# Kernel tuning notes

Measured on AMD Instinct MI355X. Metric: run time of the kernel, lower is better.

The kernel has to match this reference:

```python
import jax, jax.numpy as jnp
import numpy as np

D_K = 64
MASK_FILL = -1e9


def setup_inputs() -> dict:
    key = jax.random.key(0)
    kq, kk, kv, km = jax.random.split(key, 4)
    B, H, S, D = 2, 16, 2048, D_K
    q = jax.random.normal(kq, (B, H, S, D), dtype=jnp.float32)
    k = jax.random.normal(kk, (B, H, D, S), dtype=jnp.float32)  # pre-transposed keys
    v = jax.random.normal(kv, (B, H, S, D), dtype=jnp.float32)
    mask = jax.random.randint(km, (B, H, S, S), 0, 2).astype(jnp.bool_)
    return {"q": q, "k": k, "v": v, "mask": mask}


def reference(q, k, v, mask):
    # scores: [B, H, S, S] = q @ k (k already [B,H,D,S])
    scores = jnp.einsum("bhsd,bhdt->bhst", q, k) / jnp.sqrt(jnp.float32(D_K))
    scores = jnp.where(mask, MASK_FILL, scores)
    attn = jax.nn.softmax(scores, axis=-1)
    context = jnp.einsum("bhst,bhtd->bhsd", attn, v)
    return (context, attn)
```

## Files before the change

### kernel.cpp

```cpp
#include <hip/hip_runtime.h>

#define S_LEN    2048
#define DK       64
#define N_BH     32
#define ROWS     16
#define NTHREADS 512

typedef float          f32x4  __attribute__((ext_vector_type(4)));
typedef int            i32x4  __attribute__((ext_vector_type(4)));
typedef short          bf16x8 __attribute__((ext_vector_type(8)));
typedef unsigned short u16x8  __attribute__((ext_vector_type(8)));
typedef unsigned int   u32x4  __attribute__((ext_vector_type(4)));

__device__ __forceinline__ unsigned short f2bf(float f) {
    unsigned u = __builtin_bit_cast(unsigned, f);
    u += 0x7fffu + ((u >> 16) & 1u);
    return (unsigned short)(u >> 16);
}
__device__ __forceinline__ float bf2f(unsigned short h) {
    unsigned u = ((unsigned)h) << 16;
    return __builtin_bit_cast(float, u);
}
__device__ __forceinline__ unsigned pack_bf2(float a, float b) {
    return (unsigned)f2bf(a) | ((unsigned)f2bf(b) << 16);
}

__global__ void prep_q(const float* __restrict__ q, unsigned short* __restrict__ Q2) {
    const int bq = blockIdx.x;
    const int tx = threadIdx.x;
    const int ks = tx >> 6, g = (tx >> 4) & 3, m = tx & 15;
    const long row = ((long)(bq >> 7) * S_LEN + (bq & 127) * 16 + m);
    const float* p = q + row * DK + ks * 32 + g * 8;
    f32x4 x0 = *(const f32x4*)p, x1 = *(const f32x4*)(p + 4);
    u16x8 o;
    o[0]=f2bf(x0.x); o[1]=f2bf(x0.y); o[2]=f2bf(x0.z); o[3]=f2bf(x0.w);
    o[4]=f2bf(x1.x); o[5]=f2bf(x1.y); o[6]=f2bf(x1.z); o[7]=f2bf(x1.w);
    *(u16x8*)(Q2 + (long)bq * 1024 + tx * 8) = o;
}

__global__ void prep_k(const float* __restrict__ k, unsigned short* __restrict__ K2) {
    __shared__ float t[64][65];
    const int bh = blockIdx.x >> 5, s0 = (blockIdx.x & 31) << 6;
    const int tx = threadIdx.x;
    const float* kb = k + (long)bh * DK * S_LEN;
    #pragma unroll
    for (int i = 0; i < 16; ++i) {
        const int d = (i << 2) + (tx >> 6), s = tx & 63;
        t[d][s] = kb[(long)d * S_LEN + s0 + s];
    }
    __syncthreads();
    #pragma unroll
    for (int it = 0; it < 2; ++it) {
        const int flat = it * 256 + tx;
        const int m = flat & 15, g = (flat >> 4) & 3, ks = (flat >> 6) & 1, t16g = flat >> 7;
        const int sl = t16g * 16 + m;
        const int d0 = ks * 32 + g * 8;
        u16x8 o;
        #pragma unroll
        for (int j = 0; j < 8; ++j) o[j] = f2bf(t[d0 + j][sl]);
        const long idx = ((((long)(bh * 128 + (s0 >> 4) + t16g) * 2 + ks) * 4 + g) * 16 + m) * 8;
        *(u16x8*)(K2 + idx) = o;
    }
}

__global__ void prep_v(const float* __restrict__ v, unsigned short* __restrict__ V2) {
    __shared__ float t[64][65];
    const int bh = blockIdx.x >> 5, s0 = (blockIdx.x & 31) << 6;
    const int tx = threadIdx.x;
    #pragma unroll
    for (int i = 0; i < 16; ++i) {
        const int s = (i << 2) + (tx >> 6), d = tx & 63;
        t[s][d] = v[((long)bh * S_LEN + s0 + s) * DK + d];
    }
    __syncthreads();
    #pragma unroll
    for (int it = 0; it < 2; ++it) {
        const int flat = it * 256 + tx;
        const int d = flat & 63, tbl = flat >> 6;
        u16x8 o;
        #pragma unroll
        for (int j = 0; j < 8; ++j) o[j] = f2bf(t[tbl * 8 + j][d]);
        const long idx = (((long)(bh * 256 + (s0 >> 3) + tbl) * 64) + d) * 8;
        *(u16x8*)(V2 + idx) = o;
    }
}

template <bool WS>
__global__ __launch_bounds__(NTHREADS, 4)
void sdpa_main(const float* __restrict__ q, const float* __restrict__ k,
               const float* __restrict__ v, const int* __restrict__ mask,
               const unsigned short* __restrict__ Q2,
               const unsigned short* __restrict__ K2,
               const unsigned short* __restrict__ V2,
               float* __restrict__ ctx, float* __restrict__ attn)
{
    __shared__ float rowsum[ROWS];
    __shared__ float ctxlds[ROWS * DK];

    const int bid  = blockIdx.x;
    const int bh   = bid & (N_BH - 1);
    const int qt   = bid >> 5;
    const int tid  = threadIdx.x;
    const int wave = tid >> 6;
    const int lane = tid & 63;
    const int m    = lane & 15;
    const int g    = lane >> 4;
    const long rowbase = (long)bh * S_LEN + qt * ROWS;
    const int tw   = wave << 8;

    if (tid < ROWS) rowsum[tid] = 0.0f;
    for (int i = tid; i < ROWS * DK; i += NTHREADS) ctxlds[i] = 0.0f;
    __syncthreads();

    unsigned long long mbits = 0ull;
    {
        const int* mbase = mask + rowbase * S_LEN + tw + 4 * lane;
        #pragma unroll
        for (int r = 0; r < 16; ++r) {
            const i32x4 mk = __builtin_nontemporal_load((const i32x4*)(mbase + (long)r * S_LEN));
            const unsigned nib = (mk.x ? 1u : 0u) | (mk.y ? 2u : 0u)
                               | (mk.z ? 4u : 0u) | (mk.w ? 8u : 0u);
            mbits |= ((unsigned long long)nib) << (r * 4);
        }
    }

    bf16x8 qfrag[2];
    if (WS) {
        const unsigned short* qp = Q2 + ((long)((bh * 128 + qt) * 2) << 9) + (lane << 3);
        qfrag[0] = *(const bf16x8*)qp;
        qfrag[1] = *(const bf16x8*)(qp + 512);
    } else {
        const float* qp = q + (rowbase + m) * DK;
        #pragma unroll
        for (int ks = 0; ks < 2; ++ks) {
            const float* p = qp + ks * 32 + g * 8;
            f32x4 x0 = *(const f32x4*)p, x1 = *(const f32x4*)(p + 4);
            qfrag[ks][0]=(short)f2bf(x0.x); qfrag[ks][1]=(short)f2bf(x0.y);
            qfrag[ks][2]=(short)f2bf(x0.z); qfrag[ks][3]=(short)f2bf(x0.w);
            qfrag[ks][4]=(short)f2bf(x1.x); qfrag[ks][5]=(short)f2bf(x1.y);
            qfrag[ks][6]=(short)f2bf(x1.z); qfrag[ks][7]=(short)f2bf(x1.w);
        }
    }

    unsigned long long lanemask = 0ull;
    {
        const unsigned mlo = (unsigned)mbits, mhi = (unsigned)(mbits >> 32);
        #pragma unroll
        for (int kt = 0; kt < 8; ++kt) {
            const int sA = kt * 8 + g * 2, sB = sA + 1;
            const unsigned aLo = (unsigned)__shfl((int)mlo, sA);
            const unsigned aHi = (unsigned)__shfl((int)mhi, sA);
            const unsigned bLo = (unsigned)__shfl((int)mlo, sB);
            const unsigned bHi = (unsigned)__shfl((int)mhi, sB);
            const unsigned long long A = ((unsigned long long)aHi << 32) | aLo;
            const unsigned long long B = ((unsigned long long)bHi << 32) | bLo;
            const unsigned byt = (unsigned)((A >> (4 * m)) & 0xFull)
                               | ((unsigned)((B >> (4 * m)) & 0xFull) << 4);
            lanemask |= ((unsigned long long)byt) << (8 * kt);
        }
    }

    const int srcA = ((g & 1) << 5) + m;
    const int srcB = srcA + 16;
    const int hi   = g >> 1;

    u32x4 AF[8];
    f32x4 cacc0 = {0,0,0,0}, cacc1 = {0,0,0,0}, cacc2 = {0,0,0,0}, cacc3 = {0,0,0,0};
    float rsum = 0.0f;

    #pragma unroll
    for (int kt = 0; kt < 8; ++kt) {
        unsigned pk0e, pk1e, pk0o, pk1o;
        #pragma unroll
        for (int h = 0; h < 2; ++h) {
            f32x4 acc = {0.f, 0.f, 0.f, 0.f};
            #pragma unroll
            for (int ks = 0; ks < 2; ++ks) {
                bf16x8 kfrag;
                if (WS) {
                    const unsigned short* kp = K2
                        + (((long)(bh * 128 + wave * 16 + 2 * kt + h) * 2 + ks) << 9)
                        + (lane << 3);
                    kfrag = *(const bf16x8*)kp;
                } else {
                    const int t0 = tw + ((2 * kt + h) << 4);
                    const int tk = t0 + m;
                    const float* kp = k + (long)bh * DK * S_LEN + (long)(ks * 32 + g * 8) * S_LEN + tk;
                    #pragma unroll
                    for (int j = 0; j < 8; ++j) kfrag[j] = (short)f2bf(kp[(long)j * S_LEN]);
                }
                acc = __builtin_amdgcn_mfma_f32_16x16x32_bf16(kfrag, qfrag[ks], acc, 0, 0, 0);
            }
            const float e0 = __expf(acc[0] * 0.125f);
            const float e1 = __expf(acc[1] * 0.125f);
            const float e2 = __expf(acc[2] * 0.125f);
            const float e3 = __expf(acc[3] * 0.125f);
            if (h == 0) { pk0e = pack_bf2(e0, e1); pk1e = pack_bf2(e2, e3); }
            else        { pk0o = pack_bf2(e0, e1); pk1o = pack_bf2(e2, e3); }
        }
        const unsigned a0e = (unsigned)__shfl((int)pk0e, srcA);
        const unsigned a0o = (unsigned)__shfl((int)pk0o, srcA);
        const unsigned a1e = (unsigned)__shfl((int)pk1e, srcA);
        const unsigned a1o = (unsigned)__shfl((int)pk1o, srcA);
        const unsigned a2e = (unsigned)__shfl((int)pk0e, srcB);
        const unsigned a2o = (unsigned)__shfl((int)pk0o, srcB);
        const unsigned a3e = (unsigned)__shfl((int)pk1e, srcB);
        const unsigned a3o = (unsigned)__shfl((int)pk1o, srcB);
        u32x4 wv = { hi ? a0o : a0e, hi ? a1o : a1e,
                     hi ? a2o : a2e, hi ? a3o : a3e };
        const unsigned mb = (unsigned)(lanemask >> (8 * kt)) & 0xFFu;
        if (mb & 1u)   wv.x &= 0xFFFF0000u;
        if (mb & 2u)   wv.x &= 0x0000FFFFu;
        if (mb & 4u)   wv.y &= 0xFFFF0000u;
        if (mb & 8u)   wv.y &= 0x0000FFFFu;
        if (mb & 16u)  wv.z &= 0xFFFF0000u;
        if (mb & 32u)  wv.z &= 0x0000FFFFu;
        if (mb & 64u)  wv.w &= 0xFFFF0000u;
        if (mb & 128u) wv.w &= 0x0000FFFFu;
        AF[kt] = wv;
        rsum += ((bf2f((unsigned short)(wv.x & 0xFFFF)) + bf2f((unsigned short)(wv.x >> 16)))
               + (bf2f((unsigned short)(wv.y & 0xFFFF)) + bf2f((unsigned short)(wv.y >> 16))))
              + ((bf2f((unsigned short)(wv.z & 0xFFFF)) + bf2f((unsigned short)(wv.z >> 16)))
               + (bf2f((unsigned short)(wv.w & 0xFFFF)) + bf2f((unsigned short)(wv.w >> 16))));
        const bf16x8 af = __builtin_bit_cast(bf16x8, wv);
        #pragma unroll
        for (int dt = 0; dt < 4; ++dt) {
            bf16x8 bfv;
            if (WS) {
                const unsigned short* vp2 = V2
                    + ((((long)(bh * 256 + (wave << 5) + (kt << 2) + g)) << 6) + dt * 16 + m) * 8;
                bfv = *(const bf16x8*)vp2;
            } else {
                const int tb = tw + (kt << 5) + (g << 3);
                const float* vp = v + ((long)bh * S_LEN + tb) * DK + dt * 16 + m;
                #pragma unroll
                for (int j = 0; j < 8; ++j) bfv[j] = (short)f2bf(vp[j * DK]);
            }
            if      (dt == 0) cacc0 = __builtin_amdgcn_mfma_f32_16x16x32_bf16(af, bfv, cacc0, 0, 0, 0);
            else if (dt == 1) cacc1 = __builtin_amdgcn_mfma_f32_16x16x32_bf16(af, bfv, cacc1, 0, 0, 0);
            else if (dt == 2) cacc2 = __builtin_amdgcn_mfma_f32_16x16x32_bf16(af, bfv, cacc2, 0, 0, 0);
            else              cacc3 = __builtin_amdgcn_mfma_f32_16x16x32_bf16(af, bfv, cacc3, 0, 0, 0);
        }
    }

    rsum += __shfl_xor(rsum, 16);
    rsum += __shfl_xor(rsum, 32);
    if (lane < 16) atomicAdd(&rowsum[lane], rsum);
    #pragma unroll
    for (int i = 0; i < 4; ++i) {
        atomicAdd(&ctxlds[(4 * g + i) * DK +  0 + m], cacc0[i]);
        atomicAdd(&ctxlds[(4 * g + i) * DK + 16 + m], cacc1[i]);
        atomicAdd(&ctxlds[(4 * g + i) * DK + 32 + m], cacc2[i]);
        atomicAdd(&ctxlds[(4 * g + i) * DK + 48 + m], cacc3[i]);
    }
    __syncthreads();

    {
        const float rinv = 1.0f / rowsum[m];
        float* aout = attn + (rowbase + m) * (long)S_LEN;
        #pragma unroll
        for (int kt = 0; kt < 8; ++kt) {
            const u32x4 wv = AF[kt];
            const int tb = tw + (kt << 5) + (g << 3);
            f32x4 o0 = { bf2f((unsigned short)(wv.x & 0xFFFF)) * rinv,
                         bf2f((unsigned short)(wv.x >> 16))    * rinv,
                         bf2f((unsigned short)(wv.y & 0xFFFF)) * rinv,
                         bf2f((unsigned short)(wv.y >> 16))    * rinv };
            f32x4 o1 = { bf2f((unsigned short)(wv.z & 0xFFFF)) * rinv,
                         bf2f((unsigned short)(wv.z >> 16))    * rinv,
                         bf2f((unsigned short)(wv.w & 0xFFFF)) * rinv,
                         bf2f((unsigned short)(wv.w >> 16))    * rinv };
            __builtin_nontemporal_store(o0, (f32x4*)(aout + tb));
            __builtin_nontemporal_store(o1, (f32x4*)(aout + tb + 4));
        }
    }

    #pragma unroll
    for (int i = tid; i < ROWS * DK; i += NTHREADS) {
        const int rr = i >> 6, dd = i & 63;
        ctx[(rowbase + rr) * DK + dd] = ctxlds[i] / rowsum[rr];
    }
}

extern "C" void kernel_launch(void* const* d_in, const int* in_sizes, int n_in,
                              void* d_out, int out_size, void* d_ws, size_t ws_size,
                              hipStream_t stream)
{
    const float* q    = (const float*)d_in[0];
    const float* k    = (const float*)d_in[1];
    const float* v    = (const float*)d_in[2];
    const int*   mask = (const int*)d_in[3];

    float* ctx  = (float*)d_out;
    float* attn = ctx + (size_t)N_BH * S_LEN * DK;

    const size_t nel = (size_t)N_BH * S_LEN * DK;
    const bool use_ws = ws_size >= nel * 3 * sizeof(unsigned short);
    unsigned short* Q2 = (unsigned short*)d_ws;
    unsigned short* K2 = Q2 + nel;
    unsigned short* V2 = K2 + nel;

    const int nblocks = N_BH * (S_LEN / ROWS);

    if (use_ws) {
        prep_q<<<N_BH * 128, 128, 0, stream>>>(q, Q2);
        prep_k<<<N_BH * (S_LEN / 64), 256, 0, stream>>>(k, K2);
        prep_v<<<N_BH * (S_LEN / 64), 256, 0, stream>>>(v, V2);
        sdpa_main<true><<<nblocks, NTHREADS, 0, stream>>>(q, k, v, mask, Q2, K2, V2, ctx, attn);
    } else {
        sdpa_main<false><<<nblocks, NTHREADS, 0, stream>>>(q, k, v, mask,
                                                           nullptr, nullptr, nullptr, ctx, attn);
    }
}
```

Baseline: 459.1 us.

## Tile 128 query rows per block with LDS-staged K/V and two-pass softmax

Each block now handles 128 query rows (16 per wave) instead of 16, and streams K and V in 128-key tiles through swizzled LDS buffers with register prefetch. The first pass computes exp scores and row sums, and the second pass recomputes QK, normalises, writes attn and accumulates context. This removes the cross-wave LDS atomics and the repeated global K/V reads of the old per-wave key split. The cost is recomputing QK in the second pass, a larger LDS footprint that lowers occupancy, and more barriers. Mask bits are cached in LDS between the passes.

```diff
diff --git a/kernel.cpp b/kernel.cpp
--- a/kernel.cpp
+++ b/kernel.cpp
@@ -3,14 +3,14 @@
 #define S_LEN    2048
 #define DK       64
 #define N_BH     32
-#define ROWS     16
 #define NTHREADS 512
 
-typedef float          f32x4  __attribute__((ext_vector_type(4)));
-typedef int            i32x4  __attribute__((ext_vector_type(4)));
-typedef short          bf16x8 __attribute__((ext_vector_type(8)));
-typedef unsigned short u16x8  __attribute__((ext_vector_type(8)));
-typedef unsigned int   u32x4  __attribute__((ext_vector_type(4)));
+typedef float              f32x4  __attribute__((ext_vector_type(4)));
+typedef int                i32x4  __attribute__((ext_vector_type(4)));
+typedef short              bf16x8 __attribute__((ext_vector_type(8)));
+typedef unsigned short     u16x8  __attribute__((ext_vector_type(8)));
+typedef unsigned int       u32x4  __attribute__((ext_vector_type(4)));
+typedef unsigned long long u64;
 
 __device__ __forceinline__ unsigned short f2bf(float f) {
     unsigned u = __builtin_bit_cast(unsigned, f);
@@ -35,7 +35,7 @@
     u16x8 o;
     o[0]=f2bf(x0.x); o[1]=f2bf(x0.y); o[2]=f2bf(x0.z); o[3]=f2bf(x0.w);
     o[4]=f2bf(x1.x); o[5]=f2bf(x1.y); o[6]=f2bf(x1.z); o[7]=f2bf(x1.w);
-    *(u16x8*)(Q2 + (long)bq * 1024 + tx * 8) = o;
+    *(u16x8*)(Q2 + (long)bq * 1024 + (ks * 512) + ((g * 16 + m) * 8)) = o;
 }
 
 __global__ void prep_k(const float* __restrict__ k, unsigned short* __restrict__ K2) {
@@ -51,15 +51,15 @@
     __syncthreads();
     #pragma unroll
     for (int it = 0; it < 2; ++it) {
-        const int flat = it * 256 + tx;
-        const int m = flat & 15, g = (flat >> 4) & 3, ks = (flat >> 6) & 1, t16g = flat >> 7;
-        const int sl = t16g * 16 + m;
-        const int d0 = ks * 32 + g * 8;
+        const int f = it * 256 + tx;
+        const int tl = f >> 3, d0 = f & 7;
+        const int tg = s0 + tl;
+        const int p = tg >> 7, tp = tg & 127;
         u16x8 o;
         #pragma unroll
-        for (int j = 0; j < 8; ++j) o[j] = f2bf(t[d0 + j][sl]);
-        const long idx = ((((long)(bh * 128 + (s0 >> 4) + t16g) * 2 + ks) * 4 + g) * 16 + m) * 8;
-        *(u16x8*)(K2 + idx) = o;
+        for (int j = 0; j < 8; ++j) o[j] = f2bf(t[d0 * 8 + j][tl]);
+        const int idx = (tp * 64 + d0 * 8) ^ ((tp & 7) << 3);
+        *(u16x8*)(K2 + ((long)(bh * 16 + p) << 13) + idx) = o;
     }
 }
 
@@ -75,13 +75,15 @@
     __syncthreads();
     #pragma unroll
     for (int it = 0; it < 2; ++it) {
-        const int flat = it * 256 + tx;
-        const int d = flat & 63, tbl = flat >> 6;
+        const int f = it * 256 + tx;
+        const int d = f >> 3, t8 = (f & 7) * 8;
+        const int tg8 = s0 + t8;
+        const int p = tg8 >> 7, tp8 = tg8 & 127;
         u16x8 o;
         #pragma unroll
-        for (int j = 0; j < 8; ++j) o[j] = f2bf(t[tbl * 8 + j][d]);
-        const long idx = (((long)(bh * 256 + (s0 >> 3) + tbl) * 64) + d) * 8;
-        *(u16x8*)(V2 + idx) = o;
+        for (int j = 0; j < 8; ++j) o[j] = f2bf(t[t8 + j][d]);
+        const int idx = (d * 128 + tp8) ^ ((d & 7) << 3);
+        *(u16x8*)(V2 + ((long)(bh * 16 + p) << 13) + idx) = o;
     }
 }
 
@@ -94,8 +96,9 @@
                const unsigned short* __restrict__ V2,
                float* __restrict__ ctx, float* __restrict__ attn)
 {
-    __shared__ float rowsum[ROWS];
-    __shared__ float ctxlds[ROWS * DK];
+    __shared__ unsigned short Kbuf[8192];
+    __shared__ unsigned short Vbuf[8192];
+    __shared__ u64 Mlds[4096];
 
     const int bid  = blockIdx.x;
     const int bh   = bid & (N_BH - 1);
@@ -105,28 +108,11 @@
     const int lane = tid & 63;
     const int m    = lane & 15;
     const int g    = lane >> 4;
-    const long rowbase = (long)bh * S_LEN + qt * ROWS;
-    const int tw   = wave << 8;
-
-    if (tid < ROWS) rowsum[tid] = 0.0f;
-    for (int i = tid; i < ROWS * DK; i += NTHREADS) ctxlds[i] = 0.0f;
-    __syncthreads();
-
-    unsigned long long mbits = 0ull;
-    {
-        const int* mbase = mask + rowbase * S_LEN + tw + 4 * lane;
-        #pragma unroll
-        for (int r = 0; r < 16; ++r) {
-            const i32x4 mk = __builtin_nontemporal_load((const i32x4*)(mbase + (long)r * S_LEN));
-            const unsigned nib = (mk.x ? 1u : 0u) | (mk.y ? 2u : 0u)
-                               | (mk.z ? 4u : 0u) | (mk.w ? 8u : 0u);
-            mbits |= ((unsigned long long)nib) << (r * 4);
-        }
-    }
+    const long rowbase = (long)bh * S_LEN + qt * 128 + wave * 16;
 
     bf16x8 qfrag[2];
     if (WS) {
-        const unsigned short* qp = Q2 + ((long)((bh * 128 + qt) * 2) << 9) + (lane << 3);
+        const unsigned short* qp = Q2 + ((long)(bh * 128 + qt * 8 + wave) << 10) + (lane << 3);
         qfrag[0] = *(const bf16x8*)qp;
         qfrag[1] = *(const bf16x8*)(qp + 512);
     } else {
@@ -142,54 +128,21 @@
         }
     }
 
-    unsigned long long lanemask = 0ull;
-    {
-        const unsigned mlo = (unsigned)mbits, mhi = (unsigned)(mbits >> 32);
-        #pragma unroll
-        for (int kt = 0; kt < 8; ++kt) {
-            const int sA = kt * 8 + g * 2, sB = sA + 1;
-            const unsigned aLo = (unsigned)__shfl((int)mlo, sA);
-            const unsigned aHi = (unsigned)__shfl((int)mhi, sA);
-            const unsigned bLo = (unsigned)__shfl((int)mlo, sB);
-            const unsigned bHi = (unsigned)__shfl((int)mhi, sB);
-            const unsigned long long A = ((unsigned long long)aHi << 32) | aLo;
-            const unsigned long long B = ((unsigned long long)bHi << 32) | bLo;
-            const unsigned byt = (unsigned)((A >> (4 * m)) & 0xFull)
-                               | ((unsigned)((B >> (4 * m)) & 0xFull) << 4);
-            lanemask |= ((unsigned long long)byt) << (8 * kt);
-        }
-    }
-
     const int srcA = ((g & 1) << 5) + m;
     const int srcB = srcA + 16;
     const int hi   = g >> 1;
 
-    u32x4 AF[8];
-    f32x4 cacc0 = {0,0,0,0}, cacc1 = {0,0,0,0}, cacc2 = {0,0,0,0}, cacc3 = {0,0,0,0};
-    float rsum = 0.0f;
-
-    #pragma unroll
-    for (int kt = 0; kt < 8; ++kt) {
+    auto qk_chunk = [&](int ct16a) -> u32x4 {
         unsigned pk0e, pk1e, pk0o, pk1o;
         #pragma unroll
         for (int h = 0; h < 2; ++h) {
+            const int tl = (ct16a + h) * 16 + m;
             f32x4 acc = {0.f, 0.f, 0.f, 0.f};
             #pragma unroll
             for (int ks = 0; ks < 2; ++ks) {
-                bf16x8 kfrag;
-                if (WS) {
-                    const unsigned short* kp = K2
-                        + (((long)(bh * 128 + wave * 16 + 2 * kt + h) * 2 + ks) << 9)
-                        + (lane << 3);
-                    kfrag = *(const bf16x8*)kp;
-                } else {
-                    const int t0 = tw + ((2 * kt + h) << 4);
-                    const int tk = t0 + m;
-                    const float* kp = k + (long)bh * DK * S_LEN + (long)(ks * 32 + g * 8) * S_LEN + tk;
-                    #pragma unroll
-                    for (int j = 0; j < 8; ++j) kfrag[j] = (short)f2bf(kp[(long)j * S_LEN]);
-                }
-                acc = __builtin_amdgcn_mfma_f32_16x16x32_bf16(kfrag, qfrag[ks], acc, 0, 0, 0);
+                const int idx = (tl * 64 + ks * 32 + g * 8) ^ ((tl & 7) << 3);
+                const bf16x8 kf = *(const bf16x8*)&Kbuf[idx];
+                acc = __builtin_amdgcn_mfma_f32_16x16x32_bf16(kf, qfrag[ks], acc, 0, 0, 0);
             }
             const float e0 = __expf(acc[0] * 0.125f);
             const float e1 = __expf(acc[1] * 0.125f);
@@ -208,7 +161,10 @@
         const unsigned a3o = (unsigned)__shfl((int)pk1o, srcB);
         u32x4 wv = { hi ? a0o : a0e, hi ? a1o : a1e,
                      hi ? a2o : a2e, hi ? a3o : a3e };
-        const unsigned mb = (unsigned)(lanemask >> (8 * kt)) & 0xFFu;
+        return wv;
+    };
+
+    auto apply_mask = [&](u32x4 wv, unsigned mb) -> u32x4 {
         if (mb & 1u)   wv.x &= 0xFFFF0000u;
         if (mb & 2u)   wv.x &= 0x0000FFFFu;
         if (mb & 4u)   wv.y &= 0xFFFF0000u;
@@ -217,51 +173,176 @@
         if (mb & 32u)  wv.z &= 0x0000FFFFu;
         if (mb & 64u)  wv.w &= 0xFFFF0000u;
         if (mb & 128u) wv.w &= 0x0000FFFFu;
-        AF[kt] = wv;
-        rsum += ((bf2f((unsigned short)(wv.x & 0xFFFF)) + bf2f((unsigned short)(wv.x >> 16)))
-               + (bf2f((unsigned short)(wv.y & 0xFFFF)) + bf2f((unsigned short)(wv.y >> 16))))
-              + ((bf2f((unsigned short)(wv.z & 0xFFFF)) + bf2f((unsigned short)(wv.z >> 16)))
-               + (bf2f((unsigned short)(wv.w & 0xFFFF)) + bf2f((unsigned short)(wv.w >> 16))));
-        const bf16x8 af = __builtin_bit_cast(bf16x8, wv);
-        #pragma unroll
-        for (int dt = 0; dt < 4; ++dt) {
-            bf16x8 bfv;
+        return wv;
+    };
+
+    auto mask_burst = [&](int c) -> u64 {
+        u64 mb = 0;
+        const int* mp = mask + rowbase * (long)S_LEN + c * 256 + 4 * lane;
+        #pragma unroll
+        for (int r = 0; r < 16; ++r) {
+            const i32x4 mk = __builtin_nontemporal_load((const i32x4*)(mp + (long)r * S_LEN));
+            const unsigned nib = (mk.x ? 1u : 0u) | (mk.y ? 2u : 0u)
+                               | (mk.z ? 4u : 0u) | (mk.w ? 8u : 0u);
+            mb |= ((u64)nib) << (r * 4);
+        }
+        return mb;
+    };
+
+    auto redist = [&](u64 mbits) -> u64 {
+        u64 lm = 0;
+        const unsigned mlo = (unsigned)mbits, mhi = (unsigned)(mbits >> 32);
+        #pragma unroll
+        for (int kt = 0; kt < 8; ++kt) {
+            const int sA = kt * 8 + g * 2, sB = sA + 1;
+            const unsigned aLo = (unsigned)__shfl((int)mlo, sA);
+            const unsigned aHi = (unsigned)__shfl((int)mhi, sA);
+            const unsigned bLo = (unsigned)__shfl((int)mlo, sB);
+            const unsigned bHi = (unsigned)__shfl((int)mhi, sB);
+            const u64 A = ((u64)aHi << 32) | aLo;
+            const u64 B = ((u64)bHi << 32) | bLo;
+            const unsigned byt = (unsigned)((A >> (4 * m)) & 0xFull)
+                               | ((unsigned)((B >> (4 * m)) & 0xFull) << 4);
+            lm |= ((u64)byt) << (8 * kt);
+        }
+        return lm;
+    };
+
+    float rsum = 0.0f;
+    u64 lm = redist(mask_burst(0));
+    u16x8 kst0, kst1;
+    if (WS) {
+        const unsigned short* src = K2 + ((long)(bh * 16) << 13) + (tid << 3);
+        kst0 = *(const u16x8*)src;
+        kst1 = *(const u16x8*)(src + 4096);
+    } else {
+        const int f0 = tid, f1 = 512 + tid;
+        const int tl0 = f0 >> 3, d00 = (f0 & 7) * 8, tl1 = f1 >> 3, d01 = (f1 & 7) * 8;
+        #pragma unroll
+        for (int j = 0; j < 8; ++j) kst0[j] = f2bf(k[((long)bh * DK + d00 + j) * S_LEN + tl0]);
+        #pragma unroll
+        for (int j = 0; j < 8; ++j) kst1[j] = f2bf(k[((long)bh * DK + d01 + j) * S_LEN + tl1]);
+    }
+    for (int p = 0; p < 16; ++p) {
+        const int c = p >> 1;
+        __syncthreads();
+        {
             if (WS) {
-                const unsigned short* vp2 = V2
-                    + ((((long)(bh * 256 + (wave << 5) + (kt << 2) + g)) << 6) + dt * 16 + m) * 8;
-                bfv = *(const bf16x8*)vp2;
+                *(u16x8*)&Kbuf[tid * 8]        = kst0;
+                *(u16x8*)&Kbuf[4096 + tid * 8] = kst1;
             } else {
-                const int tb = tw + (kt << 5) + (g << 3);
-                const float* vp = v + ((long)bh * S_LEN + tb) * DK + dt * 16 + m;
-                #pragma unroll
-                for (int j = 0; j < 8; ++j) bfv[j] = (short)f2bf(vp[j * DK]);
-            }
-            if      (dt == 0) cacc0 = __builtin_amdgcn_mfma_f32_16x16x32_bf16(af, bfv, cacc0, 0, 0, 0);
-            else if (dt == 1) cacc1 = __builtin_amdgcn_mfma_f32_16x16x32_bf16(af, bfv, cacc1, 0, 0, 0);
-            else if (dt == 2) cacc2 = __builtin_amdgcn_mfma_f32_16x16x32_bf16(af, bfv, cacc2, 0, 0, 0);
-            else              cacc3 = __builtin_amdgcn_mfma_f32_16x16x32_bf16(af, bfv, cacc3, 0, 0, 0);
-        }
+                const int f0 = tid, f1 = 512 + tid;
+                const int tl0 = f0 >> 3, d00 = (f0 & 7) * 8, tl1 = f1 >> 3, d01 = (f1 & 7) * 8;
+                *(u16x8*)&Kbuf[(tl0 * 64 + d00) ^ ((tl0 & 7) << 3)] = kst0;
+                *(u16x8*)&Kbuf[(tl1 * 64 + d01) ^ ((tl1 & 7) << 3)] = kst1;
+            }
+        }
+        if (p < 15) {
+            if (WS) {
+                const unsigned short* src = K2 + ((long)(bh * 16 + p + 1) << 13) + (tid << 3);
+                kst0 = *(const u16x8*)src;
+                kst1 = *(const u16x8*)(src + 4096);
+            } else {
+                const int f0 = tid, f1 = 512 + tid;
+                const int tl0 = (p + 1) * 128 + (f0 >> 3), d00 = (f0 & 7) * 8;
+                const int tl1 = (p + 1) * 128 + (f1 >> 3), d01 = (f1 & 7) * 8;
+                #pragma unroll
+                for (int j = 0; j < 8; ++j) kst0[j] = f2bf(k[((long)bh * DK + d00 + j) * S_LEN + tl0]);
+                #pragma unroll
+                for (int j = 0; j < 8; ++j) kst1[j] = f2bf(k[((long)bh * DK + d01 + j) * S_LEN + tl1]);
+            }
+        }
+        __syncthreads();
+        if ((p & 1) == 0) Mlds[(wave << 9) + (c << 6) + lane] = lm;
+        const int b0 = (p & 1) * 4;
+        #pragma unroll
+        for (int cc = 0; cc < 4; ++cc) {
+            u32x4 wv = qk_chunk(cc * 2);
+            const unsigned mb = (unsigned)(lm >> (8 * (b0 + cc))) & 0xFFu;
+            wv = apply_mask(wv, mb);
+            rsum += ((bf2f((unsigned short)(wv.x & 0xFFFF)) + bf2f((unsigned short)(wv.x >> 16)))
+                   + (bf2f((unsigned short)(wv.y & 0xFFFF)) + bf2f((unsigned short)(wv.y >> 16))))
+                  + ((bf2f((unsigned short)(wv.z & 0xFFFF)) + bf2f((unsigned short)(wv.z >> 16)))
+                   + (bf2f((unsigned short)(wv.w & 0xFFFF)) + bf2f((unsigned short)(wv.w >> 16))));
+        }
+        if ((p & 1) == 1 && p < 15) lm = redist(mask_burst(c + 1));
     }
 
     rsum += __shfl_xor(rsum, 16);
     rsum += __shfl_xor(rsum, 32);
-    if (lane < 16) atomicAdd(&rowsum[lane], rsum);
-    #pragma unroll
-    for (int i = 0; i < 4; ++i) {
-        atomicAdd(&ctxlds[(4 * g + i) * DK +  0 + m], cacc0[i]);
-        atomicAdd(&ctxlds[(4 * g + i) * DK + 16 + m], cacc1[i]);
-        atomicAdd(&ctxlds[(4 * g + i) * DK + 32 + m], cacc2[i]);
-        atomicAdd(&ctxlds[(4 * g + i) * DK + 48 + m], cacc3[i]);
-    }
-    __syncthreads();
-
-    {
-        const float rinv = 1.0f / rowsum[m];
-        float* aout = attn + (rowbase + m) * (long)S_LEN;
-        #pragma unroll
-        for (int kt = 0; kt < 8; ++kt) {
-            const u32x4 wv = AF[kt];
-            const int tb = tw + (kt << 5) + (g << 3);
+    const float rinv = 1.0f / rsum;
+
+    f32x4 cacc0 = {0,0,0,0}, cacc1 = {0,0,0,0}, cacc2 = {0,0,0,0}, cacc3 = {0,0,0,0};
+    u16x8 vst0, vst1;
+    if (WS) {
+        const unsigned short* ks_ = K2 + ((long)(bh * 16) << 13) + (tid << 3);
+        kst0 = *(const u16x8*)ks_;  kst1 = *(const u16x8*)(ks_ + 4096);
+        const unsigned short* vs_ = V2 + ((long)(bh * 16) << 13) + (tid << 3);
+        vst0 = *(const u16x8*)vs_;  vst1 = *(const u16x8*)(vs_ + 4096);
+    } else {
+        const int f0 = tid, f1 = 512 + tid;
+        const int tl0 = f0 >> 3, d00 = (f0 & 7) * 8, tl1 = f1 >> 3, d01 = (f1 & 7) * 8;
+        #pragma unroll
+        for (int j = 0; j < 8; ++j) kst0[j] = f2bf(k[((long)bh * DK + d00 + j) * S_LEN + tl0]);
+        #pragma unroll
+        for (int j = 0; j < 8; ++j) kst1[j] = f2bf(k[((long)bh * DK + d01 + j) * S_LEN + tl1]);
+        const int dv0 = f0 >> 3, t80 = (f0 & 7) * 8, dv1 = f1 >> 3, t81 = (f1 & 7) * 8;
+        #pragma unroll
+        for (int j = 0; j < 8; ++j) vst0[j] = f2bf(v[((long)bh * S_LEN + t80 + j) * DK + dv0]);
+        #pragma unroll
+        for (int j = 0; j < 8; ++j) vst1[j] = f2bf(v[((long)bh * S_LEN + t81 + j) * DK + dv1]);
+    }
+    float* aout = attn + (rowbase + m) * (long)S_LEN;
+    for (int p = 0; p < 16; ++p) {
+        const int c = p >> 1;
+        __syncthreads();
+        {
+            if (WS) {
+                *(u16x8*)&Kbuf[tid * 8]        = kst0;
+                *(u16x8*)&Kbuf[4096 + tid * 8] = kst1;
+                *(u16x8*)&Vbuf[tid * 8]        = vst0;
+                *(u16x8*)&Vbuf[4096 + tid * 8] = vst1;
+            } else {
+                const int f0 = tid, f1 = 512 + tid;
+                const int tl0 = f0 >> 3, d00 = (f0 & 7) * 8, tl1 = f1 >> 3, d01 = (f1 & 7) * 8;
+                *(u16x8*)&Kbuf[(tl0 * 64 + d00) ^ ((tl0 & 7) << 3)] = kst0;
+                *(u16x8*)&Kbuf[(tl1 * 64 + d01) ^ ((tl1 & 7) << 3)] = kst1;
+                const int dv0 = f0 >> 3, t80 = (f0 & 7) * 8, dv1 = f1 >> 3, t81 = (f1 & 7) * 8;
+                *(u16x8*)&Vbuf[(dv0 * 128 + t80) ^ ((dv0 & 7) << 3)] = vst0;
+                *(u16x8*)&Vbuf[(dv1 * 128 + t81) ^ ((dv1 & 7) << 3)] = vst1;
+            }
+        }
+        if (p < 15) {
+            if (WS) {
+                const unsigned short* ks_ = K2 + ((long)(bh * 16 + p + 1) << 13) + (tid << 3);
+                kst0 = *(const u16x8*)ks_;  kst1 = *(const u16x8*)(ks_ + 4096);
+                const unsigned short* vs_ = V2 + ((long)(bh * 16 + p + 1) << 13) + (tid << 3);
+                vst0 = *(const u16x8*)vs_;  vst1 = *(const u16x8*)(vs_ + 4096);
+            } else {
+                const int f0 = tid, f1 = 512 + tid;
+                const int tl0 = (p+1)*128 + (f0 >> 3), d00 = (f0 & 7) * 8;
+                const int tl1 = (p+1)*128 + (f1 >> 3), d01 = (f1 & 7) * 8;
+                #pragma unroll
+                for (int j = 0; j < 8; ++j) kst0[j] = f2bf(k[((long)bh * DK + d00 + j) * S_LEN + tl0]);
+                #pragma unroll
+                for (int j = 0; j < 8; ++j) kst1[j] = f2bf(k[((long)bh * DK + d01 + j) * S_LEN + tl1]);
+                const int dv0 = f0 >> 3, t80 = (p+1)*128 + (f0 & 7) * 8;
+                const int dv1 = f1 >> 3, t81 = (p+1)*128 + (f1 & 7) * 8;
+                #pragma unroll
+                for (int j = 0; j < 8; ++j) vst0[j] = f2bf(v[((long)bh * S_LEN + t80 + j) * DK + dv0]);
+                #pragma unroll
+                for (int j = 0; j < 8; ++j) vst1[j] = f2bf(v[((long)bh * S_LEN + t81 + j) * DK + dv1]);
+            }
+        }
+        __syncthreads();
+        const u64 lm2 = Mlds[(wave << 9) + (c << 6) + lane];
+        const int b0 = (p & 1) * 4;
+        #pragma unroll
+        for (int cc = 0; cc < 4; ++cc) {
+            u32x4 wv = qk_chunk(cc * 2);
+            const unsigned mb = (unsigned)(lm2 >> (8 * (b0 + cc))) & 0xFFu;
+            wv = apply_mask(wv, mb);
+            const int tb = p * 128 + cc * 32 + g * 8;
             f32x4 o0 = { bf2f((unsigned short)(wv.x & 0xFFFF)) * rinv,
                          bf2f((unsigned short)(wv.x >> 16))    * rinv,
                          bf2f((unsigned short)(wv.y & 0xFFFF)) * rinv,
@@ -272,13 +353,28 @@
                          bf2f((unsigned short)(wv.w >> 16))    * rinv };
             __builtin_nontemporal_store(o0, (f32x4*)(aout + tb));
             __builtin_nontemporal_store(o1, (f32x4*)(aout + tb + 4));
+            const bf16x8 af = __builtin_bit_cast(bf16x8, wv);
+            #pragma unroll
+            for (int dt = 0; dt < 4; ++dt) {
+                const int d = dt * 16 + m;
+                const int idx = (d * 128 + cc * 32 + g * 8) ^ ((d & 7) << 3);
+                const bf16x8 bfv = *(const bf16x8*)&Vbuf[idx];
+                if      (dt == 0) cacc0 = __builtin_amdgcn_mfma_f32_16x16x32_bf16(af, bfv, cacc0, 0, 0, 0);
+                else if (dt == 1) cacc1 = __builtin_amdgcn_mfma_f32_16x16x32_bf16(af, bfv, cacc1, 0, 0, 0);
+                else if (dt == 2) cacc2 = __builtin_amdgcn_mfma_f32_16x16x32_bf16(af, bfv, cacc2, 0, 0, 0);
+                else              cacc3 = __builtin_amdgcn_mfma_f32_16x16x32_bf16(af, bfv, cacc3, 0, 0, 0);
+            }
         }
     }
 
     #pragma unroll
-    for (int i = tid; i < ROWS * DK; i += NTHREADS) {
-        const int rr = i >> 6, dd = i & 63;
-        ctx[(rowbase + rr) * DK + dd] = ctxlds[i] / rowsum[rr];
+    for (int i = 0; i < 4; ++i) {
+        const float ri = __shfl(rinv, 4 * g + i);
+        float* cp = ctx + (rowbase + 4 * g + i) * DK + m;
+        cp[ 0] = cacc0[i] * ri;
+        cp[16] = cacc1[i] * ri;
+        cp[32] = cacc2[i] * ri;
+        cp[48] = cacc3[i] * ri;
     }
 }
 
@@ -300,7 +396,7 @@
     unsigned short* K2 = Q2 + nel;
     unsigned short* V2 = K2 + nel;
 
-    const int nblocks = N_BH * (S_LEN / ROWS);
+    const int nblocks = N_BH * (S_LEN / 128);
 
     if (use_ws) {
         prep_q<<<N_BH * 128, 128, 0, stream>>>(q, Q2);
```

New measurement: 565.0 us. 1.23x slower.

## Two-pass softmax: recompute QK scores to stream attn output, drop Q prep kernel

Applied to the files above, without the earlier changes.

Splits the main kernel into two passes. The first computes QK^T and exp only to get row sums. The second recomputes the scores and writes normalized attention straight out while doing the PV MFMAs, so the bf16 probabilities no longer sit in registers (AF[8]) until the end. Masking is now applied before exp using a per-tile shuffle of the mask bits, and the separate prep_q launch is removed by converting Q inside the kernel. The cost is double the QK MFMA and exp work plus extra K2 reads, in exchange for lower register pressure and the attn stores overlapping with compute.

```diff
diff --git a/kernel.cpp b/kernel.cpp
--- a/kernel.cpp
+++ b/kernel.cpp
@@ -23,19 +23,6 @@
 }
 __device__ __forceinline__ unsigned pack_bf2(float a, float b) {
     return (unsigned)f2bf(a) | ((unsigned)f2bf(b) << 16);
-}
-
-__global__ void prep_q(const float* __restrict__ q, unsigned short* __restrict__ Q2) {
-    const int bq = blockIdx.x;
-    const int tx = threadIdx.x;
-    const int ks = tx >> 6, g = (tx >> 4) & 3, m = tx & 15;
-    const long row = ((long)(bq >> 7) * S_LEN + (bq & 127) * 16 + m);
-    const float* p = q + row * DK + ks * 32 + g * 8;
-    f32x4 x0 = *(const f32x4*)p, x1 = *(const f32x4*)(p + 4);
-    u16x8 o;
-    o[0]=f2bf(x0.x); o[1]=f2bf(x0.y); o[2]=f2bf(x0.z); o[3]=f2bf(x0.w);
-    o[4]=f2bf(x1.x); o[5]=f2bf(x1.y); o[6]=f2bf(x1.z); o[7]=f2bf(x1.w);
-    *(u16x8*)(Q2 + (long)bq * 1024 + tx * 8) = o;
 }
 
 __global__ void prep_k(const float* __restrict__ k, unsigned short* __restrict__ K2) {
@@ -89,13 +76,11 @@
 __global__ __launch_bounds__(NTHREADS, 4)
 void sdpa_main(const float* __restrict__ q, const float* __restrict__ k,
                const float* __restrict__ v, const int* __restrict__ mask,
-               const unsigned short* __restrict__ Q2,
                const unsigned short* __restrict__ K2,
                const unsigned short* __restrict__ V2,
                float* __restrict__ ctx, float* __restrict__ attn)
 {
     __shared__ float rowsum[ROWS];
-    __shared__ float ctxlds[ROWS * DK];
 
     const int bid  = blockIdx.x;
     const int bh   = bid & (N_BH - 1);
@@ -109,10 +94,8 @@
     const int tw   = wave << 8;
 
     if (tid < ROWS) rowsum[tid] = 0.0f;
-    for (int i = tid; i < ROWS * DK; i += NTHREADS) ctxlds[i] = 0.0f;
-    __syncthreads();
-
-    unsigned long long mbits = 0ull;
+
+    unsigned mlo = 0, mhi = 0;
     {
         const int* mbase = mask + rowbase * S_LEN + tw + 4 * lane;
         #pragma unroll
@@ -120,16 +103,13 @@
             const i32x4 mk = __builtin_nontemporal_load((const i32x4*)(mbase + (long)r * S_LEN));
             const unsigned nib = (mk.x ? 1u : 0u) | (mk.y ? 2u : 0u)
                                | (mk.z ? 4u : 0u) | (mk.w ? 8u : 0u);
-            mbits |= ((unsigned long long)nib) << (r * 4);
+            if (r < 8) mlo |= nib << (r * 4);
+            else       mhi |= nib << ((r - 8) * 4);
         }
     }
 
     bf16x8 qfrag[2];
-    if (WS) {
-        const unsigned short* qp = Q2 + ((long)((bh * 128 + qt) * 2) << 9) + (lane << 3);
-        qfrag[0] = *(const bf16x8*)qp;
-        qfrag[1] = *(const bf16x8*)(qp + 512);
-    } else {
+    {
         const float* qp = q + (rowbase + m) * DK;
         #pragma unroll
         for (int ks = 0; ks < 2; ++ks) {
@@ -142,62 +122,61 @@
         }
     }
 
-    unsigned long long lanemask = 0ull;
-    {
-        const unsigned mlo = (unsigned)mbits, mhi = (unsigned)(mbits >> 32);
-        #pragma unroll
-        for (int kt = 0; kt < 8; ++kt) {
-            const int sA = kt * 8 + g * 2, sB = sA + 1;
-            const unsigned aLo = (unsigned)__shfl((int)mlo, sA);
-            const unsigned aHi = (unsigned)__shfl((int)mhi, sA);
-            const unsigned bLo = (unsigned)__shfl((int)mlo, sB);
-            const unsigned bHi = (unsigned)__shfl((int)mhi, sB);
-            const unsigned long long A = ((unsigned long long)aHi << 32) | aLo;
-            const unsigned long long B = ((unsigned long long)bHi << 32) | bLo;
-            const unsigned byt = (unsigned)((A >> (4 * m)) & 0xFull)
-                               | ((unsigned)((B >> (4 * m)) & 0xFull) << 4);
-            lanemask |= ((unsigned long long)byt) << (8 * kt);
-        }
-    }
+    auto qk_tile = [&](int ct) -> f32x4 {
+        f32x4 acc = {0.f, 0.f, 0.f, 0.f};
+        #pragma unroll
+        for (int ks = 0; ks < 2; ++ks) {
+            bf16x8 kfrag;
+            if (WS) {
+                const unsigned short* kp = K2
+                    + (((long)(bh * 128 + wave * 16 + ct) * 2 + ks) << 9)
+                    + (lane << 3);
+                kfrag = *(const bf16x8*)kp;
+            } else {
+                const int tk = tw + ct * 16 + m;
+                const float* kp = k + (long)bh * DK * S_LEN + (long)(ks * 32 + g * 8) * S_LEN + tk;
+                #pragma unroll
+                for (int j = 0; j < 8; ++j) kfrag[j] = (short)f2bf(kp[(long)j * S_LEN]);
+            }
+            acc = __builtin_amdgcn_mfma_f32_16x16x32_bf16(kfrag, qfrag[ks], acc, 0, 0, 0);
+        }
+        const int sL = ct * 4 + g;
+        const unsigned a = (unsigned)__shfl((int)mlo, sL);
+        const unsigned b = (unsigned)__shfl((int)mhi, sL);
+        const unsigned nib = (((m & 8) ? b : a) >> ((m & 7) * 4)) & 0xFu;
+        f32x4 e;
+        e.x = (nib & 1u) ? 0.0f : __expf(acc[0] * 0.125f);
+        e.y = (nib & 2u) ? 0.0f : __expf(acc[1] * 0.125f);
+        e.z = (nib & 4u) ? 0.0f : __expf(acc[2] * 0.125f);
+        e.w = (nib & 8u) ? 0.0f : __expf(acc[3] * 0.125f);
+        return e;
+    };
+
+    float rsum = 0.0f;
+    #pragma unroll
+    for (int ct = 0; ct < 16; ++ct) {
+        const f32x4 e = qk_tile(ct);
+        rsum += (e.x + e.y) + (e.z + e.w);
+    }
+    rsum += __shfl_xor(rsum, 16);
+    rsum += __shfl_xor(rsum, 32);
+    __syncthreads();
+    if (lane < 16) atomicAdd(&rowsum[lane], rsum);
+    __syncthreads();
+    const float rinv = 1.0f / rowsum[m];
 
     const int srcA = ((g & 1) << 5) + m;
     const int srcB = srcA + 16;
     const int hi   = g >> 1;
-
-    u32x4 AF[8];
     f32x4 cacc0 = {0,0,0,0}, cacc1 = {0,0,0,0}, cacc2 = {0,0,0,0}, cacc3 = {0,0,0,0};
-    float rsum = 0.0f;
+    float* aout = attn + (rowbase + m) * (long)S_LEN;
 
     #pragma unroll
     for (int kt = 0; kt < 8; ++kt) {
-        unsigned pk0e, pk1e, pk0o, pk1o;
-        #pragma unroll
-        for (int h = 0; h < 2; ++h) {
-            f32x4 acc = {0.f, 0.f, 0.f, 0.f};
-            #pragma unroll
-            for (int ks = 0; ks < 2; ++ks) {
-                bf16x8 kfrag;
-                if (WS) {
-                    const unsigned short* kp = K2
-                        + (((long)(bh * 128 + wave * 16 + 2 * kt + h) * 2 + ks) << 9)
-                        + (lane << 3);
-                    kfrag = *(const bf16x8*)kp;
-                } else {
-                    const int t0 = tw + ((2 * kt + h) << 4);
-                    const int tk = t0 + m;
-                    const float* kp = k + (long)bh * DK * S_LEN + (long)(ks * 32 + g * 8) * S_LEN + tk;
-                    #pragma unroll
-                    for (int j = 0; j < 8; ++j) kfrag[j] = (short)f2bf(kp[(long)j * S_LEN]);
-                }
-                acc = __builtin_amdgcn_mfma_f32_16x16x32_bf16(kfrag, qfrag[ks], acc, 0, 0, 0);
-            }
-            const float e0 = __expf(acc[0] * 0.125f);
-            const float e1 = __expf(acc[1] * 0.125f);
-            const float e2 = __expf(acc[2] * 0.125f);
-            const float e3 = __expf(acc[3] * 0.125f);
-            if (h == 0) { pk0e = pack_bf2(e0, e1); pk1e = pack_bf2(e2, e3); }
-            else        { pk0o = pack_bf2(e0, e1); pk1o = pack_bf2(e2, e3); }
-        }
+        const f32x4 ee = qk_tile(2 * kt);
+        const f32x4 eo = qk_tile(2 * kt + 1);
+        const unsigned pk0e = pack_bf2(ee.x, ee.y), pk1e = pack_bf2(ee.z, ee.w);
+        const unsigned pk0o = pack_bf2(eo.x, eo.y), pk1o = pack_bf2(eo.z, eo.w);
         const unsigned a0e = (unsigned)__shfl((int)pk0e, srcA);
         const unsigned a0o = (unsigned)__shfl((int)pk0o, srcA);
         const unsigned a1e = (unsigned)__shfl((int)pk1e, srcA);
@@ -206,22 +185,19 @@
         const unsigned a2o = (unsigned)__shfl((int)pk0o, srcB);
         const unsigned a3e = (unsigned)__shfl((int)pk1e, srcB);
         const unsigned a3o = (unsigned)__shfl((int)pk1o, srcB);
-        u32x4 wv = { hi ? a0o : a0e, hi ? a1o : a1e,
-                     hi ? a2o : a2e, hi ? a3o : a3e };
-        const unsigned mb = (unsigned)(lanemask >> (8 * kt)) & 0xFFu;
-        if (mb & 1u)   wv.x &= 0xFFFF0000u;
-        if (mb & 2u)   wv.x &= 0x0000FFFFu;
-        if (mb & 4u)   wv.y &= 0xFFFF0000u;
-        if (mb & 8u)   wv.y &= 0x0000FFFFu;
-        if (mb & 16u)  wv.z &= 0xFFFF0000u;
-        if (mb & 32u)  wv.z &= 0x0000FFFFu;
-        if (mb & 64u)  wv.w &= 0xFFFF0000u;
-        if (mb & 128u) wv.w &= 0x0000FFFFu;
-        AF[kt] = wv;
-        rsum += ((bf2f((unsigned short)(wv.x & 0xFFFF)) + bf2f((unsigned short)(wv.x >> 16)))
-               + (bf2f((unsigned short)(wv.y & 0xFFFF)) + bf2f((unsigned short)(wv.y >> 16))))
-              + ((bf2f((unsigned short)(wv.z & 0xFFFF)) + bf2f((unsigned short)(wv.z >> 16)))
-               + (bf2f((unsigned short)(wv.w & 0xFFFF)) + bf2f((unsigned short)(wv.w >> 16))));
+        const u32x4 wv = { hi ? a0o : a0e, hi ? a1o : a1e,
+                           hi ? a2o : a2e, hi ? a3o : a3e };
+        const int tb = tw + (kt << 5) + (g << 3);
+        f32x4 o0 = { bf2f((unsigned short)(wv.x & 0xFFFF)) * rinv,
+                     bf2f((unsigned short)(wv.x >> 16))    * rinv,
+                     bf2f((unsigned short)(wv.y & 0xFFFF)) * rinv,
+                     bf2f((unsigned short)(wv.y >> 16))    * rinv };
+        f32x4 o1 = { bf2f((unsigned short)(wv.z & 0xFFFF)) * rinv,
+                     bf2f((unsigned short)(wv.z >> 16))    * rinv,
+                     bf2f((unsigned short)(wv.w & 0xFFFF)) * rinv,
+                     bf2f((unsigned short)(wv.w >> 16))    * rinv };
+        __builtin_nontemporal_store(o0, (f32x4*)(aout + tb));
+        __builtin_nontemporal_store(o1, (f32x4*)(aout + tb + 4));
         const bf16x8 af = __builtin_bit_cast(bf16x8, wv);
         #pragma unroll
         for (int dt = 0; dt < 4; ++dt) {
@@ -231,7 +207,6 @@
                     + ((((long)(bh * 256 + (wave << 5) + (kt << 2) + g)) << 6) + dt * 16 + m) * 8;
                 bfv = *(const bf16x8*)vp2;
             } else {
-                const int tb = tw + (kt << 5) + (g << 3);
                 const float* vp = v + ((long)bh * S_LEN + tb) * DK + dt * 16 + m;
                 #pragma unroll
                 for (int j = 0; j < 8; ++j) bfv[j] = (short)f2bf(vp[j * DK]);
@@ -243,9 +218,9 @@
         }
     }
 
-    rsum += __shfl_xor(rsum, 16);
-    rsum += __shfl_xor(rsum, 32);
-    if (lane < 16) atomicAdd(&rowsum[lane], rsum);
+    __shared__ float ctxlds[ROWS * DK];
+    for (int i = tid; i < ROWS * DK; i += NTHREADS) ctxlds[i] = 0.0f;
+    __syncthreads();
     #pragma unroll
     for (int i = 0; i < 4; ++i) {
         atomicAdd(&ctxlds[(4 * g + i) * DK +  0 + m], cacc0[i]);
@@ -254,28 +229,6 @@
         atomicAdd(&ctxlds[(4 * g + i) * DK + 48 + m], cacc3[i]);
     }
     __syncthreads();
-
-    {
-        const float rinv = 1.0f / rowsum[m];
-        float* aout = attn + (rowbase + m) * (long)S_LEN;
-        #pragma unroll
-        for (int kt = 0; kt < 8; ++kt) {
-            const u32x4 wv = AF[kt];
-            const int tb = tw + (kt << 5) + (g << 3);
-            f32x4 o0 = { bf2f((unsigned short)(wv.x & 0xFFFF)) * rinv,
-                         bf2f((unsigned short)(wv.x >> 16))    * rinv,
-                         bf2f((unsigned short)(wv.y & 0xFFFF)) * rinv,
-                         bf2f((unsigned short)(wv.y >> 16))    * rinv };
-            f32x4 o1 = { bf2f((unsigned short)(wv.z & 0xFFFF)) * rinv,
-                         bf2f((unsigned short)(wv.z >> 16))    * rinv,
-                         bf2f((unsigned short)(wv.w & 0xFFFF)) * rinv,
-                         bf2f((unsigned short)(wv.w >> 16))    * rinv };
-            __builtin_nontemporal_store(o0, (f32x4*)(aout + tb));
-            __builtin_nontemporal_store(o1, (f32x4*)(aout + tb + 4));
-        }
-    }
-
-    #pragma unroll
     for (int i = tid; i < ROWS * DK; i += NTHREADS) {
         const int rr = i >> 6, dd = i & 63;
         ctx[(rowbase + rr) * DK + dd] = ctxlds[i] / rowsum[rr];
@@ -295,20 +248,18 @@
     float* attn = ctx + (size_t)N_BH * S_LEN * DK;
 
     const size_t nel = (size_t)N_BH * S_LEN * DK;
-    const bool use_ws = ws_size >= nel * 3 * sizeof(unsigned short);
-    unsigned short* Q2 = (unsigned short*)d_ws;
-    unsigned short* K2 = Q2 + nel;
+    const bool use_ws = ws_size >= nel * 2 * sizeof(unsigned short);
+    unsigned short* K2 = (unsigned short*)d_ws;
     unsigned short* V2 = K2 + nel;
 
     const int nblocks = N_BH * (S_LEN / ROWS);
 
     if (use_ws) {
-        prep_q<<<N_BH * 128, 128, 0, stream>>>(q, Q2);
         prep_k<<<N_BH * (S_LEN / 64), 256, 0, stream>>>(k, K2);
         prep_v<<<N_BH * (S_LEN / 64), 256, 0, stream>>>(v, V2);
-        sdpa_main<true><<<nblocks, NTHREADS, 0, stream>>>(q, k, v, mask, Q2, K2, V2, ctx, attn);
+        sdpa_main<true><<<nblocks, NTHREADS, 0, stream>>>(q, k, v, mask, K2, V2, ctx, attn);
     } else {
         sdpa_main<false><<<nblocks, NTHREADS, 0, stream>>>(q, k, v, mask,
-                                                           nullptr, nullptr, nullptr, ctx, attn);
-    }
-}
+                                                           nullptr, nullptr, ctx, attn);
+    }
+}
```

Result: slower. 501.4 us (+9.2%).
